# Optimization experiments

Measured on AMD Instinct MI355X. Metric: run time of the kernel, lower is better.

## Reference

```python
import jax, jax.numpy as jnp
import numpy as np

N_NODES = 100000
N_EDGES = 3200000
D_FEAT = 64
ALPHA = 0.1
K_STEPS = 10


def setup_inputs() -> dict:
    key = jax.random.key(0)
    k1, k2, k3, k4 = jax.random.split(key, 4)
    x = jax.random.normal(k1, (N_NODES, D_FEAT), dtype=jnp.float32)
    edge_row = jax.random.randint(k2, (N_EDGES,), 0, N_NODES, dtype=jnp.int32)
    edge_col = jax.random.randint(k3, (N_EDGES,), 0, N_NODES, dtype=jnp.int32)
    edge_weight = jax.random.uniform(k4, (N_EDGES,), dtype=jnp.float32)
    return {"x": x, "edge_row": edge_row, "edge_col": edge_col, "edge_weight": edge_weight}


def reference(x, edge_row, edge_col, edge_weight):
    # APPNP propagation: h <- (1-alpha) * A @ h + alpha * x, repeated K times.
    # A is sparse [N, N] given as an edge list; A @ h done via gather + segment_sum.
    def spmm(h):
        msgs = edge_weight[:, None] * h[edge_col]          # [E, d]
        return jax.ops.segment_sum(msgs, edge_row, num_segments=N_NODES)  # [N, d]

    h = x
    for _ in range(K_STEPS):
        h = (1.0 - ALPHA) * spmm(h) + ALPHA * x
    return h
```

## Files before the change

### kernel.cpp

```cpp
#include <hip/hip_runtime.h>

typedef unsigned int u32;
typedef unsigned long long u64;
typedef u32   v4u __attribute__((ext_vector_type(4)));
typedef float v4f __attribute__((ext_vector_type(4)));

#define NN 100000
#define NE 3200000
#define DF 64
#define ALPHA 0.1f
#define BETA 0.9f
#define K_STEPS 10
#define NBKT 782
#define EPT 16
#define CHUNK (256 * EPT)
#define NCHB ((NE + CHUNK - 1) / CHUNK)

__device__ __forceinline__ u32 rne_bf16(float f) {
    u32 u = __float_as_uint(f);
    return (u + 0x7FFFu + ((u >> 16) & 1u)) >> 16;
}
__device__ __forceinline__ float bf_lo(u32 w) { return __uint_as_float(w << 16); }
__device__ __forceinline__ float bf_hi(u32 w) { return __uint_as_float(w & 0xFFFF0000u); }

__global__ void bucket_hist(const int* __restrict__ row, int* __restrict__ bcnt) {
    __shared__ int s[NBKT];
    for (int i = threadIdx.x; i < NBKT; i += 256) s[i] = 0;
    __syncthreads();
    int base = blockIdx.x * CHUNK + threadIdx.x;
    #pragma unroll
    for (int j = 0; j < EPT; ++j) {
        int e = base + j * 256;
        if (e < NE) atomicAdd(&s[row[e] >> 7], 1);
    }
    __syncthreads();
    for (int i = threadIdx.x; i < NBKT; i += 256) {
        int v = s[i];
        if (v) atomicAdd(&bcnt[i], v);
    }
}

__global__ void scan_buckets(const int* __restrict__ bcnt, int* __restrict__ bbase,
                             int* __restrict__ bcur) {
    __shared__ int s[1024];
    int i = threadIdx.x;
    int v = (i < NBKT) ? bcnt[i] : 0;
    s[i] = v;
    __syncthreads();
    for (int off = 1; off < 1024; off <<= 1) {
        int t = (i >= off) ? s[i - off] : 0;
        __syncthreads();
        s[i] += t;
        __syncthreads();
    }
    if (i < NBKT) { int b = s[i] - v; bbase[i] = b; bcur[i] = b; }
}

__global__ void bucket_scatter(const int* __restrict__ row, const int* __restrict__ col,
                               const float* __restrict__ w, int* __restrict__ bcur,
                               u64* __restrict__ e64) {
    __shared__ int scnt[NBKT];
    __shared__ int sbase[NBKT];
    for (int i = threadIdx.x; i < NBKT; i += 256) scnt[i] = 0;
    __syncthreads();
    int base = blockIdx.x * CHUNK + threadIdx.x;
    int rows[EPT];
    #pragma unroll
    for (int j = 0; j < EPT; ++j) {
        int e = base + j * 256;
        int r = (e < NE) ? row[e] : -1;
        rows[j] = r;
        if (r >= 0) atomicAdd(&scnt[r >> 7], 1);
    }
    __syncthreads();
    for (int i = threadIdx.x; i < NBKT; i += 256) {
        int c = scnt[i];
        sbase[i] = c ? atomicAdd(&bcur[i], c) : 0;
    }
    __syncthreads();
    for (int i = threadIdx.x; i < NBKT; i += 256) scnt[i] = 0;
    __syncthreads();
    #pragma unroll
    for (int j = 0; j < EPT; ++j) {
        int e = base + j * 256;
        int r = rows[j];
        if (r >= 0) {
            int b = r >> 7;
            int rank = atomicAdd(&scnt[b], 1);
            u32 cw = ((u32)col[e] << 15) | (rne_bf16(w[e]) & 0x7FFFu);
            e64[sbase[b] + rank] = ((u64)(r & 127) << 32) | cw;
        }
    }
}

__global__ void build_rows(const u64* __restrict__ e64, const int* __restrict__ bcnt,
                           const int* __restrict__ bbase, u32* __restrict__ edgesF,
                           int* __restrict__ rp) {
    __shared__ int rc[128];
    __shared__ int rb[128];
    int b = blockIdx.x;
    int cnt = bcnt[b], base = bbase[b];
    if (threadIdx.x < 128) rc[threadIdx.x] = 0;
    __syncthreads();
    for (int e = threadIdx.x; e < cnt; e += 256)
        atomicAdd(&rc[(int)(e64[base + e] >> 32)], 1);
    __syncthreads();
    if (threadIdx.x < 128) rb[threadIdx.x] = rc[threadIdx.x];
    __syncthreads();
    for (int off = 1; off < 128; off <<= 1) {
        int t = (threadIdx.x < 128 && threadIdx.x >= off) ? rb[threadIdx.x - off] : 0;
        __syncthreads();
        if (threadIdx.x < 128) rb[threadIdx.x] += t;
        __syncthreads();
    }
    if (threadIdx.x < 128) {
        int r = b * 128 + threadIdx.x;
        if (r < NN) rp[r] = base + rb[threadIdx.x];
        rc[threadIdx.x] = rb[threadIdx.x] - rc[threadIdx.x];
    }
    __syncthreads();
    for (int e = threadIdx.x; e < cnt; e += 256) {
        u64 ent = e64[base + e];
        int pos = atomicAdd(&rc[(int)(ent >> 32)], 1);
        edgesF[base + pos] = (u32)ent;
    }
}

__global__ void conv_x(const float* __restrict__ x, u32* __restrict__ xb) {
    int t = blockIdx.x * blockDim.x + threadIdx.x;
    if (t >= NN * 8) return;
    const float4* src = (const float4*)(x + (size_t)t * 8);
    float4 a = src[0], b = src[1];
    uint4 o;
    o.x = rne_bf16(a.x) | (rne_bf16(a.y) << 16);
    o.y = rne_bf16(a.z) | (rne_bf16(a.w) << 16);
    o.z = rne_bf16(b.x) | (rne_bf16(b.y) << 16);
    o.w = rne_bf16(b.z) | (rne_bf16(b.w) << 16);
    *(uint4*)(xb + (size_t)t * 4) = o;
}

__global__ __launch_bounds__(256) void
gather_step(const int* __restrict__ rp, const u32* __restrict__ edges,
            const u32* __restrict__ h, const u32* __restrict__ xb,
            u32* __restrict__ hn, float* __restrict__ outf, int final_step) {
    int lane = threadIdx.x & 63;
    int node = blockIdx.x * 4 + (threadIdx.x >> 6);
    int slice = lane >> 3;
    int fg = lane & 7;

    int start = (node == 0) ? 0 : rp[node - 1];
    int end = rp[node];

    float a0=0.f,a1=0.f,a2=0.f,a3=0.f,a4=0.f,a5=0.f,a6=0.f,a7=0.f;
    #pragma unroll 2
    for (int e = start + slice; e < end; e += 8) {
        u32 ew = __builtin_nontemporal_load(edges + e);
        u32 c = ew >> 15;
        float wv = __uint_as_float((ew & 0x7FFFu) << 16);
        const uint4 hv = *(const uint4*)(h + ((size_t)c << 5) + (fg << 2));
        a0 += wv * bf_lo(hv.x); a1 += wv * bf_hi(hv.x);
        a2 += wv * bf_lo(hv.y); a3 += wv * bf_hi(hv.y);
        a4 += wv * bf_lo(hv.z); a5 += wv * bf_hi(hv.z);
        a6 += wv * bf_lo(hv.w); a7 += wv * bf_hi(hv.w);
    }
    for (int m = 8; m <= 32; m <<= 1) {
        a0 += __shfl_xor(a0, m, 64); a1 += __shfl_xor(a1, m, 64);
        a2 += __shfl_xor(a2, m, 64); a3 += __shfl_xor(a3, m, 64);
        a4 += __shfl_xor(a4, m, 64); a5 += __shfl_xor(a5, m, 64);
        a6 += __shfl_xor(a6, m, 64); a7 += __shfl_xor(a7, m, 64);
    }
    uint4 xv = *(const uint4*)(xb + ((size_t)node << 5) + (fg << 2));
    float o0 = BETA * a0 + ALPHA * bf_lo(xv.x);
    float o1 = BETA * a1 + ALPHA * bf_hi(xv.x);
    float o2 = BETA * a2 + ALPHA * bf_lo(xv.y);
    float o3 = BETA * a3 + ALPHA * bf_hi(xv.y);
    float o4 = BETA * a4 + ALPHA * bf_lo(xv.z);
    float o5 = BETA * a5 + ALPHA * bf_hi(xv.z);
    float o6 = BETA * a6 + ALPHA * bf_lo(xv.w);
    float o7 = BETA * a7 + ALPHA * bf_hi(xv.w);

    if (!final_step) {
        if (slice == 0) {
            v4u o;
            o.x = rne_bf16(o0) | (rne_bf16(o1) << 16);
            o.y = rne_bf16(o2) | (rne_bf16(o3) << 16);
            o.z = rne_bf16(o4) | (rne_bf16(o5) << 16);
            o.w = rne_bf16(o6) | (rne_bf16(o7) << 16);
            __builtin_nontemporal_store(o, (v4u*)(hn + ((size_t)node << 5) + (fg << 2)));
        }
    } else {
        if (slice < 2) {
            v4f v;
            if (slice) { v.x = o4; v.y = o5; v.z = o6; v.w = o7; }
            else       { v.x = o0; v.y = o1; v.z = o2; v.w = o3; }
            __builtin_nontemporal_store(v, (v4f*)(outf + (size_t)node * DF + fg * 8 + slice * 4));
        }
    }
}


extern "C" void kernel_launch(void* const* d_in, const int* in_sizes, int n_in,
                              void* d_out, int out_size, void* d_ws, size_t ws_size,
                              hipStream_t stream) {
    const float* x    = (const float*)d_in[0];
    const int*   erow = (const int*)  d_in[1];
    const int*   ecol = (const int*)  d_in[2];
    const float* ew   = (const float*)d_in[3];
    float* out = (float*)d_out;

    char* ws = (char*)d_ws;
    u32* edgesF = (u32*)(ws);
    u32* xb     = (u32*)(ws + 12800000);
    u32* hA     = (u32*)(ws + 25600000);
    u32* hB     = (u32*)(ws + 38400000);
    u64* e64    = (u64*)(ws + 25600000);
    int* rp     = (int*)(ws + 51200000);
    int* bcnt   = (int*)(ws + 51600000);
    int* bbase  = (int*)(ws + 51604096);
    int* bcur   = (int*)(ws + 51608192);

    dim3 blk(256);
    dim3 gChunk(NCHB);
    dim3 gConv((NN * 8 + 255) / 256);
    dim3 gG(NN / 4);

    (void)hipMemsetAsync(bcnt, 0, NBKT * sizeof(int), stream);
    bucket_hist<<<gChunk, blk, 0, stream>>>(erow, bcnt);
    scan_buckets<<<1, 1024, 0, stream>>>(bcnt, bbase, bcur);
    bucket_scatter<<<gChunk, blk, 0, stream>>>(erow, ecol, ew, bcur, e64);
    build_rows<<<NBKT, blk, 0, stream>>>(e64, bcnt, bbase, edgesF, rp);
    conv_x<<<gConv, blk, 0, stream>>>(x, xb);

    for (int k = 0; k < K_STEPS; ++k) {
        const u32* src = (k == 0) ? xb : ((k & 1) ? hA : hB);
        u32* dst = (k & 1) ? hB : hA;
        int fin = (k == K_STEPS - 1);
        gather_step<<<gG, blk, 0, stream>>>(rp, edgesF, src, xb,
                                            fin ? nullptr : dst,
                                            fin ? out : nullptr, fin);
    }
}
```

Baseline: 864.4 us.

## Replace two-level bucket sort with direct per-row histogram and atomic scatter CSR build

The CSR build now does a per-row global atomic histogram, a three-kernel multi-block prefix scan, and a direct scatter where each edge takes its slot with a global atomicAdd on its row cursor. This removes the bucketed two-pass sort and the 64-bit intermediate edge array, saving a full pass over the edges. The cost is heavy global atomic traffic: 3.2M atomics in each of two passes, spread over 100K addresses. Edge order within a row becomes nondeterministic, which changes the float summation order.

```diff
diff --git a/kernel.cpp b/kernel.cpp
--- a/kernel.cpp
+++ b/kernel.cpp
@@ -11,10 +11,11 @@
 #define ALPHA 0.1f
 #define BETA 0.9f
 #define K_STEPS 10
-#define NBKT 782
-#define EPT 16
-#define CHUNK (256 * EPT)
-#define NCHB ((NE + CHUNK - 1) / CHUNK)
+
+#define EPTE 8
+#define EB   (256 * EPTE)
+#define NEB  ((NE + EB - 1) / EB)
+#define NSCB ((NN + 1023) / 1024)
 
 __device__ __forceinline__ u32 rne_bf16(float f) {
     u32 u = __float_as_uint(f);
@@ -23,106 +24,71 @@
 __device__ __forceinline__ float bf_lo(u32 w) { return __uint_as_float(w << 16); }
 __device__ __forceinline__ float bf_hi(u32 w) { return __uint_as_float(w & 0xFFFF0000u); }
 
-__global__ void bucket_hist(const int* __restrict__ row, int* __restrict__ bcnt) {
-    __shared__ int s[NBKT];
-    for (int i = threadIdx.x; i < NBKT; i += 256) s[i] = 0;
+__global__ void row_hist(const int* __restrict__ row, int* __restrict__ rcnt) {
+    int base = blockIdx.x * EB + threadIdx.x;
+    #pragma unroll
+    for (int j = 0; j < EPTE; ++j) {
+        int e = base + j * 256;
+        if (e < NE) atomicAdd(&rcnt[row[e]], 1);
+    }
+}
+
+__global__ void scan_a(const int* __restrict__ rcnt, int* __restrict__ rtmp,
+                       int* __restrict__ rpart) {
+    __shared__ int s[1024];
+    int i = blockIdx.x * 1024 + threadIdx.x;
+    int v = (i < NN) ? rcnt[i] : 0;
+    s[threadIdx.x] = v;
     __syncthreads();
-    int base = blockIdx.x * CHUNK + threadIdx.x;
-    #pragma unroll
-    for (int j = 0; j < EPT; ++j) {
-        int e = base + j * 256;
-        if (e < NE) atomicAdd(&s[row[e] >> 7], 1);
-    }
-    __syncthreads();
-    for (int i = threadIdx.x; i < NBKT; i += 256) {
-        int v = s[i];
-        if (v) atomicAdd(&bcnt[i], v);
-    }
-}
-
-__global__ void scan_buckets(const int* __restrict__ bcnt, int* __restrict__ bbase,
-                             int* __restrict__ bcur) {
-    __shared__ int s[1024];
+    for (int off = 1; off < 1024; off <<= 1) {
+        int t = (threadIdx.x >= off) ? s[threadIdx.x - off] : 0;
+        __syncthreads();
+        s[threadIdx.x] += t;
+        __syncthreads();
+    }
+    if (i < NN) rtmp[i] = s[threadIdx.x];
+    if (threadIdx.x == 1023) rpart[blockIdx.x] = s[1023];
+}
+
+__global__ void scan_b(int* __restrict__ rpart) {
+    __shared__ int s[128];
     int i = threadIdx.x;
-    int v = (i < NBKT) ? bcnt[i] : 0;
+    int v = (i < NSCB) ? rpart[i] : 0;
     s[i] = v;
     __syncthreads();
-    for (int off = 1; off < 1024; off <<= 1) {
+    for (int off = 1; off < 128; off <<= 1) {
         int t = (i >= off) ? s[i - off] : 0;
         __syncthreads();
         s[i] += t;
         __syncthreads();
     }
-    if (i < NBKT) { int b = s[i] - v; bbase[i] = b; bcur[i] = b; }
-}
-
-__global__ void bucket_scatter(const int* __restrict__ row, const int* __restrict__ col,
-                               const float* __restrict__ w, int* __restrict__ bcur,
-                               u64* __restrict__ e64) {
-    __shared__ int scnt[NBKT];
-    __shared__ int sbase[NBKT];
-    for (int i = threadIdx.x; i < NBKT; i += 256) scnt[i] = 0;
-    __syncthreads();
-    int base = blockIdx.x * CHUNK + threadIdx.x;
-    int rows[EPT];
+    if (i < NSCB) rpart[i] = s[i] - v;
+}
+
+__global__ void scan_c(const int* __restrict__ rtmp, const int* __restrict__ rpart,
+                       const int* __restrict__ rcnt, int* __restrict__ rp,
+                       int* __restrict__ rcur) {
+    int i = blockIdx.x * 256 + threadIdx.x;
+    if (i < NN) {
+        int inc = rtmp[i] + rpart[i >> 10];
+        rp[i] = inc;
+        rcur[i] = inc - rcnt[i];
+    }
+}
+
+__global__ void scatter_edges(const int* __restrict__ row, const int* __restrict__ col,
+                              const float* __restrict__ w, int* __restrict__ rcur,
+                              u32* __restrict__ edgesF) {
+    int base = blockIdx.x * EB + threadIdx.x;
     #pragma unroll
-    for (int j = 0; j < EPT; ++j) {
+    for (int j = 0; j < EPTE; ++j) {
         int e = base + j * 256;
-        int r = (e < NE) ? row[e] : -1;
-        rows[j] = r;
-        if (r >= 0) atomicAdd(&scnt[r >> 7], 1);
-    }
-    __syncthreads();
-    for (int i = threadIdx.x; i < NBKT; i += 256) {
-        int c = scnt[i];
-        sbase[i] = c ? atomicAdd(&bcur[i], c) : 0;
-    }
-    __syncthreads();
-    for (int i = threadIdx.x; i < NBKT; i += 256) scnt[i] = 0;
-    __syncthreads();
-    #pragma unroll
-    for (int j = 0; j < EPT; ++j) {
-        int e = base + j * 256;
-        int r = rows[j];
-        if (r >= 0) {
-            int b = r >> 7;
-            int rank = atomicAdd(&scnt[b], 1);
+        if (e < NE) {
+            int r = row[e];
             u32 cw = ((u32)col[e] << 15) | (rne_bf16(w[e]) & 0x7FFFu);
-            e64[sbase[b] + rank] = ((u64)(r & 127) << 32) | cw;
+            int pos = atomicAdd(&rcur[r], 1);
+            edgesF[pos] = cw;
         }
-    }
-}
-
-__global__ void build_rows(const u64* __restrict__ e64, const int* __restrict__ bcnt,
-                           const int* __restrict__ bbase, u32* __restrict__ edgesF,
-                           int* __restrict__ rp) {
-    __shared__ int rc[128];
-    __shared__ int rb[128];
-    int b = blockIdx.x;
-    int cnt = bcnt[b], base = bbase[b];
-    if (threadIdx.x < 128) rc[threadIdx.x] = 0;
-    __syncthreads();
-    for (int e = threadIdx.x; e < cnt; e += 256)
-        atomicAdd(&rc[(int)(e64[base + e] >> 32)], 1);
-    __syncthreads();
-    if (threadIdx.x < 128) rb[threadIdx.x] = rc[threadIdx.x];
-    __syncthreads();
-    for (int off = 1; off < 128; off <<= 1) {
-        int t = (threadIdx.x < 128 && threadIdx.x >= off) ? rb[threadIdx.x - off] : 0;
-        __syncthreads();
-        if (threadIdx.x < 128) rb[threadIdx.x] += t;
-        __syncthreads();
-    }
-    if (threadIdx.x < 128) {
-        int r = b * 128 + threadIdx.x;
-        if (r < NN) rp[r] = base + rb[threadIdx.x];
-        rc[threadIdx.x] = rb[threadIdx.x] - rc[threadIdx.x];
-    }
-    __syncthreads();
-    for (int e = threadIdx.x; e < cnt; e += 256) {
-        u64 ent = e64[base + e];
-        int pos = atomicAdd(&rc[(int)(ent >> 32)], 1);
-        edgesF[base + pos] = (u32)ent;
     }
 }
 
@@ -213,22 +179,23 @@
     u32* xb     = (u32*)(ws + 12800000);
     u32* hA     = (u32*)(ws + 25600000);
     u32* hB     = (u32*)(ws + 38400000);
-    u64* e64    = (u64*)(ws + 25600000);
     int* rp     = (int*)(ws + 51200000);
-    int* bcnt   = (int*)(ws + 51600000);
-    int* bbase  = (int*)(ws + 51604096);
-    int* bcur   = (int*)(ws + 51608192);
+    int* rcnt   = (int*)(ws + 25600000);
+    int* rtmp   = (int*)(ws + 26000000);
+    int* rcur   = (int*)(ws + 26400000);
+    int* rpart  = (int*)(ws + 26800000);
 
     dim3 blk(256);
-    dim3 gChunk(NCHB);
+    dim3 gE(NEB);
     dim3 gConv((NN * 8 + 255) / 256);
     dim3 gG(NN / 4);
 
-    (void)hipMemsetAsync(bcnt, 0, NBKT * sizeof(int), stream);
-    bucket_hist<<<gChunk, blk, 0, stream>>>(erow, bcnt);
-    scan_buckets<<<1, 1024, 0, stream>>>(bcnt, bbase, bcur);
-    bucket_scatter<<<gChunk, blk, 0, stream>>>(erow, ecol, ew, bcur, e64);
-    build_rows<<<NBKT, blk, 0, stream>>>(e64, bcnt, bbase, edgesF, rp);
+    (void)hipMemsetAsync(rcnt, 0, NN * sizeof(int), stream);
+    row_hist<<<gE, blk, 0, stream>>>(erow, rcnt);
+    scan_a<<<dim3(NSCB), dim3(1024), 0, stream>>>(rcnt, rtmp, rpart);
+    scan_b<<<dim3(1), dim3(128), 0, stream>>>(rpart);
+    scan_c<<<dim3((NN + 255) / 256), blk, 0, stream>>>(rtmp, rpart, rcnt, rp, rcur);
+    scatter_edges<<<gE, blk, 0, stream>>>(erow, ecol, ew, rcur, edgesF);
     conv_x<<<gConv, blk, 0, stream>>>(x, xb);
 
     for (int k = 0; k < K_STEPS; ++k) {
```

Measured after the change: 1.115 ms. 29.0% more time.

## Sort edges within each row by column range to improve gather locality

Applied to the files above, without the earlier changes.

The bucket scatter now packs a sort key made of the local row and the top three bits of the column index. build_rows runs with 1024 threads and counting-sorts on that key, so the edges of each row come out grouped by column range. This should make the feature gathers more local in cache across the ten propagation steps. The gather loop unroll also goes from 2 to 4 to raise memory-level parallelism, at the cost of extra setup work in build_rows, a 1024-entry shared scan, and more register pressure.

```diff
diff --git a/kernel.cpp b/kernel.cpp
--- a/kernel.cpp
+++ b/kernel.cpp
@@ -15,6 +15,7 @@
 #define EPT 16
 #define CHUNK (256 * EPT)
 #define NCHB ((NE + CHUNK - 1) / CHUNK)
+#define NKEY 1024
 
 __device__ __forceinline__ u32 rne_bf16(float f) {
     u32 u = __float_as_uint(f);
@@ -87,39 +88,43 @@
         if (r >= 0) {
             int b = r >> 7;
             int rank = atomicAdd(&scnt[b], 1);
-            u32 cw = ((u32)col[e] << 15) | (rne_bf16(w[e]) & 0x7FFFu);
-            e64[sbase[b] + rank] = ((u64)(r & 127) << 32) | cw;
+            u32 c = (u32)col[e];
+            u32 cw = (c << 15) | (rne_bf16(w[e]) & 0x7FFFu);
+            u32 key = ((u32)(r & 127) << 3) | (c >> 14);
+            e64[sbase[b] + rank] = ((u64)key << 32) | cw;
         }
     }
 }
 
-__global__ void build_rows(const u64* __restrict__ e64, const int* __restrict__ bcnt,
-                           const int* __restrict__ bbase, u32* __restrict__ edgesF,
-                           int* __restrict__ rp) {
-    __shared__ int rc[128];
-    __shared__ int rb[128];
+__global__ __launch_bounds__(1024) void
+build_rows(const u64* __restrict__ e64, const int* __restrict__ bcnt,
+           const int* __restrict__ bbase, u32* __restrict__ edgesF,
+           int* __restrict__ rp) {
+    __shared__ int rc[NKEY];
+    __shared__ int rb[NKEY];
     int b = blockIdx.x;
+    int tid = threadIdx.x;
     int cnt = bcnt[b], base = bbase[b];
-    if (threadIdx.x < 128) rc[threadIdx.x] = 0;
-    __syncthreads();
-    for (int e = threadIdx.x; e < cnt; e += 256)
+    rc[tid] = 0;
+    __syncthreads();
+    for (int e = tid; e < cnt; e += 1024)
         atomicAdd(&rc[(int)(e64[base + e] >> 32)], 1);
     __syncthreads();
-    if (threadIdx.x < 128) rb[threadIdx.x] = rc[threadIdx.x];
-    __syncthreads();
-    for (int off = 1; off < 128; off <<= 1) {
-        int t = (threadIdx.x < 128 && threadIdx.x >= off) ? rb[threadIdx.x - off] : 0;
-        __syncthreads();
-        if (threadIdx.x < 128) rb[threadIdx.x] += t;
-        __syncthreads();
-    }
-    if (threadIdx.x < 128) {
-        int r = b * 128 + threadIdx.x;
-        if (r < NN) rp[r] = base + rb[threadIdx.x];
-        rc[threadIdx.x] = rb[threadIdx.x] - rc[threadIdx.x];
-    }
-    __syncthreads();
-    for (int e = threadIdx.x; e < cnt; e += 256) {
+    rb[tid] = rc[tid];
+    __syncthreads();
+    for (int off = 1; off < 1024; off <<= 1) {
+        int t = (tid >= off) ? rb[tid - off] : 0;
+        __syncthreads();
+        rb[tid] += t;
+        __syncthreads();
+    }
+    if ((tid & 7) == 7) {
+        int r = b * 128 + (tid >> 3);
+        if (r < NN) rp[r] = base + rb[tid];
+    }
+    rc[tid] = rb[tid] - rc[tid];
+    __syncthreads();
+    for (int e = tid; e < cnt; e += 1024) {
         u64 ent = e64[base + e];
         int pos = atomicAdd(&rc[(int)(ent >> 32)], 1);
         edgesF[base + pos] = (u32)ent;
@@ -152,7 +157,7 @@
     int end = rp[node];
 
     float a0=0.f,a1=0.f,a2=0.f,a3=0.f,a4=0.f,a5=0.f,a6=0.f,a7=0.f;
-    #pragma unroll 2
+    #pragma unroll 4
     for (int e = start + slice; e < end; e += 8) {
         u32 ew = __builtin_nontemporal_load(edges + e);
         u32 c = ew >> 15;
@@ -228,7 +233,7 @@
     bucket_hist<<<gChunk, blk, 0, stream>>>(erow, bcnt);
     scan_buckets<<<1, 1024, 0, stream>>>(bcnt, bbase, bcur);
     bucket_scatter<<<gChunk, blk, 0, stream>>>(erow, ecol, ew, bcur, e64);
-    build_rows<<<NBKT, blk, 0, stream>>>(e64, bcnt, bbase, edgesF, rp);
+    build_rows<<<NBKT, dim3(1024), 0, stream>>>(e64, bcnt, bbase, edgesF, rp);
     conv_x<<<gConv, blk, 0, stream>>>(x, xb);
 
     for (int k = 0; k < K_STEPS; ++k) {
```

Result: no change. 872.2 us (+0.9%).

## Split feature dimension into four quarter-planes to shrink gather working set

Applied to the files above, without the earlier changes.

Stores node features as four separate planes of 16 bf16 features each, and launches one block group per quarter. Each gather pass then only touches a 3.2 MB plane instead of the full 12.8 MB table, so random row gathers should fit better in L2/LLC. The cost is that edge lists and row pointers are read four times per step, and each lane now loads 4 bytes instead of 16 bytes per edge, which means more load instructions.

```diff
diff --git a/kernel.cpp b/kernel.cpp
--- a/kernel.cpp
+++ b/kernel.cpp
@@ -4,6 +4,7 @@
 typedef unsigned long long u64;
 typedef u32   v4u __attribute__((ext_vector_type(4)));
 typedef float v4f __attribute__((ext_vector_type(4)));
+typedef float v2f __attribute__((ext_vector_type(2)));
 
 #define NN 100000
 #define NE 3200000
@@ -15,6 +16,8 @@
 #define EPT 16
 #define CHUNK (256 * EPT)
 #define NCHB ((NE + CHUNK - 1) / CHUNK)
+#define NQB 25000
+#define QSTRIDE 800000
 
 __device__ __forceinline__ u32 rne_bf16(float f) {
     u32 u = __float_as_uint(f);
@@ -126,74 +129,68 @@
     }
 }
 
-__global__ void conv_x(const float* __restrict__ x, u32* __restrict__ xb) {
+__global__ void conv_xq(const float* __restrict__ x, u32* __restrict__ xq) {
     int t = blockIdx.x * blockDim.x + threadIdx.x;
-    if (t >= NN * 8) return;
-    const float4* src = (const float4*)(x + (size_t)t * 8);
-    float4 a = src[0], b = src[1];
-    uint4 o;
-    o.x = rne_bf16(a.x) | (rne_bf16(a.y) << 16);
-    o.y = rne_bf16(a.z) | (rne_bf16(a.w) << 16);
-    o.z = rne_bf16(b.x) | (rne_bf16(b.y) << 16);
-    o.w = rne_bf16(b.z) | (rne_bf16(b.w) << 16);
-    *(uint4*)(xb + (size_t)t * 4) = o;
+    if (t >= NN * 4) return;
+    int node = t >> 2;
+    int q = t & 3;
+    const float4* src = (const float4*)(x + (size_t)node * DF + q * 16);
+    float4 a = src[0], b = src[1], c = src[2], d = src[3];
+    uint4 o0, o1;
+    o0.x = rne_bf16(a.x) | (rne_bf16(a.y) << 16);
+    o0.y = rne_bf16(a.z) | (rne_bf16(a.w) << 16);
+    o0.z = rne_bf16(b.x) | (rne_bf16(b.y) << 16);
+    o0.w = rne_bf16(b.z) | (rne_bf16(b.w) << 16);
+    o1.x = rne_bf16(c.x) | (rne_bf16(c.y) << 16);
+    o1.y = rne_bf16(c.z) | (rne_bf16(c.w) << 16);
+    o1.z = rne_bf16(d.x) | (rne_bf16(d.y) << 16);
+    o1.w = rne_bf16(d.z) | (rne_bf16(d.w) << 16);
+    u32* dst = xq + (size_t)q * QSTRIDE + ((size_t)node << 3);
+    *(uint4*)(dst) = o0;
+    *(uint4*)(dst + 4) = o1;
 }
 
 __global__ __launch_bounds__(256) void
-gather_step(const int* __restrict__ rp, const u32* __restrict__ edges,
-            const u32* __restrict__ h, const u32* __restrict__ xb,
-            u32* __restrict__ hn, float* __restrict__ outf, int final_step) {
+gather_q(const int* __restrict__ rp, const u32* __restrict__ edges,
+         const u32* __restrict__ h, const u32* __restrict__ xq,
+         u32* __restrict__ hn, float* __restrict__ outf, int final_step) {
+    int bx = blockIdx.x;
+    int q  = bx / NQB;
+    int nb = bx - q * NQB;
     int lane = threadIdx.x & 63;
-    int node = blockIdx.x * 4 + (threadIdx.x >> 6);
+    int node = nb * 4 + (threadIdx.x >> 6);
     int slice = lane >> 3;
     int fg = lane & 7;
 
+    const u32* hq = h + (size_t)q * QSTRIDE;
+
     int start = (node == 0) ? 0 : rp[node - 1];
     int end = rp[node];
 
-    float a0=0.f,a1=0.f,a2=0.f,a3=0.f,a4=0.f,a5=0.f,a6=0.f,a7=0.f;
-    #pragma unroll 2
+    float a0 = 0.f, a1 = 0.f;
+    #pragma unroll 4
     for (int e = start + slice; e < end; e += 8) {
         u32 ew = __builtin_nontemporal_load(edges + e);
         u32 c = ew >> 15;
         float wv = __uint_as_float((ew & 0x7FFFu) << 16);
-        const uint4 hv = *(const uint4*)(h + ((size_t)c << 5) + (fg << 2));
-        a0 += wv * bf_lo(hv.x); a1 += wv * bf_hi(hv.x);
-        a2 += wv * bf_lo(hv.y); a3 += wv * bf_hi(hv.y);
-        a4 += wv * bf_lo(hv.z); a5 += wv * bf_hi(hv.z);
-        a6 += wv * bf_lo(hv.w); a7 += wv * bf_hi(hv.w);
+        u32 hv = hq[((size_t)c << 3) + fg];
+        a0 += wv * bf_lo(hv);
+        a1 += wv * bf_hi(hv);
     }
     for (int m = 8; m <= 32; m <<= 1) {
-        a0 += __shfl_xor(a0, m, 64); a1 += __shfl_xor(a1, m, 64);
-        a2 += __shfl_xor(a2, m, 64); a3 += __shfl_xor(a3, m, 64);
-        a4 += __shfl_xor(a4, m, 64); a5 += __shfl_xor(a5, m, 64);
-        a6 += __shfl_xor(a6, m, 64); a7 += __shfl_xor(a7, m, 64);
-    }
-    uint4 xv = *(const uint4*)(xb + ((size_t)node << 5) + (fg << 2));
-    float o0 = BETA * a0 + ALPHA * bf_lo(xv.x);
-    float o1 = BETA * a1 + ALPHA * bf_hi(xv.x);
-    float o2 = BETA * a2 + ALPHA * bf_lo(xv.y);
-    float o3 = BETA * a3 + ALPHA * bf_hi(xv.y);
-    float o4 = BETA * a4 + ALPHA * bf_lo(xv.z);
-    float o5 = BETA * a5 + ALPHA * bf_hi(xv.z);
-    float o6 = BETA * a6 + ALPHA * bf_lo(xv.w);
-    float o7 = BETA * a7 + ALPHA * bf_hi(xv.w);
-
-    if (!final_step) {
-        if (slice == 0) {
-            v4u o;
-            o.x = rne_bf16(o0) | (rne_bf16(o1) << 16);
-            o.y = rne_bf16(o2) | (rne_bf16(o3) << 16);
-            o.z = rne_bf16(o4) | (rne_bf16(o5) << 16);
-            o.w = rne_bf16(o6) | (rne_bf16(o7) << 16);
-            __builtin_nontemporal_store(o, (v4u*)(hn + ((size_t)node << 5) + (fg << 2)));
-        }
-    } else {
-        if (slice < 2) {
-            v4f v;
-            if (slice) { v.x = o4; v.y = o5; v.z = o6; v.w = o7; }
-            else       { v.x = o0; v.y = o1; v.z = o2; v.w = o3; }
-            __builtin_nontemporal_store(v, (v4f*)(outf + (size_t)node * DF + fg * 8 + slice * 4));
+        a0 += __shfl_xor(a0, m, 64);
+        a1 += __shfl_xor(a1, m, 64);
+    }
+    if (slice == 0) {
+        u32 xv = xq[(size_t)q * QSTRIDE + ((size_t)node << 3) + fg];
+        float o0 = BETA * a0 + ALPHA * bf_lo(xv);
+        float o1 = BETA * a1 + ALPHA * bf_hi(xv);
+        if (!final_step) {
+            u32 o = rne_bf16(o0) | (rne_bf16(o1) << 16);
+            __builtin_nontemporal_store(o, hn + (size_t)q * QSTRIDE + ((size_t)node << 3) + fg);
+        } else {
+            v2f v; v.x = o0; v.y = o1;
+            __builtin_nontemporal_store(v, (v2f*)(outf + (size_t)node * DF + q * 16 + fg * 2));
         }
     }
 }
@@ -210,7 +207,7 @@
 
     char* ws = (char*)d_ws;
     u32* edgesF = (u32*)(ws);
-    u32* xb     = (u32*)(ws + 12800000);
+    u32* xq     = (u32*)(ws + 12800000);
     u32* hA     = (u32*)(ws + 25600000);
     u32* hB     = (u32*)(ws + 38400000);
     u64* e64    = (u64*)(ws + 25600000);
@@ -221,22 +218,22 @@
 
     dim3 blk(256);
     dim3 gChunk(NCHB);
-    dim3 gConv((NN * 8 + 255) / 256);
-    dim3 gG(NN / 4);
+    dim3 gConv((NN * 4 + 255) / 256);
+    dim3 gG(4 * NQB);
 
     (void)hipMemsetAsync(bcnt, 0, NBKT * sizeof(int), stream);
     bucket_hist<<<gChunk, blk, 0, stream>>>(erow, bcnt);
     scan_buckets<<<1, 1024, 0, stream>>>(bcnt, bbase, bcur);
     bucket_scatter<<<gChunk, blk, 0, stream>>>(erow, ecol, ew, bcur, e64);
     build_rows<<<NBKT, blk, 0, stream>>>(e64, bcnt, bbase, edgesF, rp);
-    conv_x<<<gConv, blk, 0, stream>>>(x, xb);
+    conv_xq<<<gConv, blk, 0, stream>>>(x, xq);
 
     for (int k = 0; k < K_STEPS; ++k) {
-        const u32* src = (k == 0) ? xb : ((k & 1) ? hA : hB);
+        const u32* src = (k == 0) ? xq : ((k & 1) ? hA : hB);
         u32* dst = (k & 1) ? hB : hA;
         int fin = (k == K_STEPS - 1);
-        gather_step<<<gG, blk, 0, stream>>>(rp, edgesF, src, xb,
-                                            fin ? nullptr : dst,
-                                            fin ? out : nullptr, fin);
-    }
-}
+        gather_q<<<gG, blk, 0, stream>>>(rp, edgesF, src, xq,
+                                         fin ? nullptr : dst,
+                                         fin ? out : nullptr, fin);
+    }
+}
```

Measured after the change: 2.185 ms. 153% more time.
